# Kernel optimization log

Hardware: AMD Instinct MI355X
Metric: run time of the kernel (lower is better)

## Reference

```python
import jax, jax.numpy as jnp
import numpy as np

NUM_BINS = 64
MAX_DIST = 25.0
HIDDEN = 256
B = 64        # number of graphs
S = 1024      # points per graph (setup builds equal-size contiguous segments)
EPS = 1e-8


def setup_inputs() -> dict:
    key = jax.random.key(0)
    k1, k2, k3, k4, k5 = jax.random.split(key, 5)
    N = B * S
    # scale positions so pairwise distances spread across [0, 25] bins
    pos = jax.random.normal(k1, (N, 3), dtype=jnp.float32) * 5.0
    batch = jnp.repeat(jnp.arange(B, dtype=jnp.int32), S)  # sorted graph ids
    # nn.Linear params, torch convention W:[out,in]
    W1 = jax.random.normal(k2, (HIDDEN, NUM_BINS), dtype=jnp.float32) / np.sqrt(NUM_BINS)
    b1 = jax.random.normal(k3, (HIDDEN,), dtype=jnp.float32) * 0.01
    W2 = jax.random.normal(k4, (HIDDEN, HIDDEN), dtype=jnp.float32) / np.sqrt(HIDDEN)
    b2 = jax.random.normal(k5, (HIDDEN,), dtype=jnp.float32) * 0.01
    return {"pos": pos, "W1": W1, "b1": b1, "W2": W2, "b2": b2, "batch": batch}


def _histograms(pos, batch):
    # batch ids are contiguous equal-size segments -> reshape into [B,S,3]
    p = pos.reshape(B, S, 3)
    # pairwise distances per graph via gram trick (matches torch.cdist)
    sq = jnp.sum(p * p, axis=-1)                                  # [B,S]
    d2 = sq[:, :, None] + sq[:, None, :] - 2.0 * jnp.einsum("bsd,btd->bst", p, p)
    dist = jnp.sqrt(jnp.maximum(d2, 0.0))                         # [B,S,S]
    triu = jnp.triu(jnp.ones((S, S), dtype=bool), k=1)            # i<j pairs
    # histc semantics: values in [0, MAX_DIST] counted, value==MAX_DIST -> last bin
    valid = triu[None] & (dist <= MAX_DIST)
    bins = jnp.clip(jnp.floor(dist * (NUM_BINS / MAX_DIST)).astype(jnp.int32), 0, NUM_BINS - 1)
    ids = (jnp.arange(B, dtype=jnp.int32)[:, None, None] * NUM_BINS + bins).reshape(-1)
    hist = jax.ops.segment_sum(valid.astype(jnp.float32).reshape(-1), ids,
                               num_segments=B * NUM_BINS).reshape(B, NUM_BINS)
    return hist / (jnp.sum(hist, axis=-1, keepdims=True) + EPS)


def reference(pos, W1, b1, W2, b2, batch):
    hist = _histograms(pos, batch)                                # [B, NUM_BINS]
    h = jax.nn.silu(hist @ W1.T + b1)                             # [B, HIDDEN]
    return h @ W2.T + b2                                          # [B, HIDDEN]
```

## Files before the change

### kernel.cpp

```cpp
#include <hip/hip_runtime.h>

#define NBINS 64
#define NGRAPH 64
#define SPTS 1024
#define HID 256
#define TILE 128
#define NPAIR 36
#define BPG NPAIR
#define NSUB 8
#define NBINT 65

__device__ __constant__ unsigned char ti_tab[NPAIR] = {
  0,0,0,0,0,0,0,0, 1,1,1,1,1,1,1, 2,2,2,2,2,2, 3,3,3,3,3, 4,4,4,4, 5,5,5, 6,6, 7};
__device__ __constant__ unsigned char tj_tab[NPAIR] = {
  0,1,2,3,4,5,6,7, 1,2,3,4,5,6,7, 2,3,4,5,6,7, 3,4,5,6,7, 4,5,6,7, 5,6,7, 6,7, 7};

template <bool OFFDIAG>
__device__ __forceinline__ void pair_loop(const float4* __restrict__ plj,
                                          unsigned int* __restrict__ h8,
                                          float4 pa, float4 pb, int il0, int il1,
                                          int jbase, unsigned int sub) {
  #pragma unroll 8
  for (int jj = 0; jj < 32; ++jj) {
    int jl = jbase + jj;
    float4 pj = plj[jl];
    float dxa = pa.x - pj.x, dya = pa.y - pj.y, dza = pa.z - pj.z;
    float d2a = dxa * dxa + dya * dya + dza * dza;
    float dxb = pb.x - pj.x, dyb = pb.y - pj.y, dzb = pb.z - pj.z;
    float d2b = dxb * dxb + dyb * dyb + dzb * dzb;
    unsigned int ia = (unsigned int)(int)__builtin_amdgcn_sqrtf(d2a);
    unsigned int ib = (unsigned int)(int)__builtin_amdgcn_sqrtf(d2b);
    ia = ia > 64u ? 64u : ia;
    ib = ib > 64u ? 64u : ib;
    if (!OFFDIAG) {
      ia = (il0 < jl) ? ia : 64u;
      ib = (il1 < jl) ? ib : 64u;
    }
    atomicAdd(&h8[ia * NSUB + sub], 1u);
    atomicAdd(&h8[ib * NSUB + sub], 1u);
  }
}

__global__ __launch_bounds__(256) void hist_kernel(const float* __restrict__ pos,
                                                   unsigned int* __restrict__ partial) {
  int bid = blockIdx.x;
  int g   = bid / NPAIR;
  int p   = bid - g * NPAIR;
  int ti  = ti_tab[p];
  int tj  = tj_tab[p];
  int t   = threadIdx.x;
  const float S = 2.56f;

  __shared__ float4 plj[TILE];
  __shared__ unsigned int h8[NBINT * NSUB];

  h8[t] = 0u;
  h8[t + 256] = 0u;
  if (t < NBINT * NSUB - 512) h8[t + 512] = 0u;
  if (t < TILE) {
    const float* gp = pos + (size_t)((g << 10) + (tj << 7) + t) * 3;
    plj[t] = make_float4(gp[0] * S, gp[1] * S, gp[2] * S, 0.0f);
  }

  int il0 = (t & 63) * 2;
  int il1 = il0 + 1;
  const float* ip = pos + (size_t)((g << 10) + (ti << 7) + il0) * 3;
  float4 pa = make_float4(ip[0] * S, ip[1] * S, ip[2] * S, 0.0f);
  float4 pb = make_float4(ip[3] * S, ip[4] * S, ip[5] * S, 0.0f);
  int jbase = (t >> 6) * 32;
  unsigned int sub = t & (NSUB - 1);
  __syncthreads();

  if (ti != tj) pair_loop<true >(plj, h8, pa, pb, il0, il1, jbase, sub);
  else          pair_loop<false>(plj, h8, pa, pb, il0, il1, jbase, sub);
  __syncthreads();

  if (t < NBINS) {
    unsigned int s = 0u;
    #pragma unroll
    for (int k = 0; k < NSUB; ++k) s += h8[t * NSUB + k];
    partial[(size_t)bid * NBINS + t] = s;
  }
}

__global__ __launch_bounds__(256) void mlp_kernel(const unsigned int* __restrict__ partial,
                                                  const float* __restrict__ W1,
                                                  const float* __restrict__ b1,
                                                  const float* __restrict__ W2,
                                                  const float* __restrict__ b2,
                                                  float* __restrict__ out) {
  int g = blockIdx.x >> 2;
  int q = blockIdx.x & 3;
  int t = threadIdx.x;
  __shared__ float hn[NBINS];
  __shared__ float h1[HID];
  __shared__ float p2[4][NBINS];

  if (t < NBINS) {
    unsigned int s = 0u;
    const unsigned int* pp = partial + (size_t)g * BPG * NBINS + t;
    #pragma unroll
    for (int p = 0; p < BPG; ++p) s += pp[p * NBINS];
    float hv = (float)s;
    float tot = hv;
    #pragma unroll
    for (int m = 1; m < 64; m <<= 1) tot += __shfl_xor(tot, m, 64);
    hn[t] = hv / (tot + 1e-8f);
  }
  __syncthreads();

  {
    float acc = b1[t];
    const float4* w = (const float4*)(W1 + (size_t)t * NBINS);
    #pragma unroll
    for (int k = 0; k < NBINS / 4; ++k) {
      float4 wv = w[k];
      acc += hn[4 * k] * wv.x + hn[4 * k + 1] * wv.y +
             hn[4 * k + 2] * wv.z + hn[4 * k + 3] * wv.w;
    }
    float sig = 1.0f / (1.0f + expf(-acc));
    h1[t] = acc * sig;
  }
  __syncthreads();

  {
    int o  = (q << 6) + (t & 63);
    int ks = (t >> 6) << 6;
    float acc = 0.0f;
    const float4* w = (const float4*)(W2 + (size_t)o * HID + ks);
    #pragma unroll
    for (int k = 0; k < 16; ++k) {
      float4 wv = w[k];
      acc += h1[ks + 4 * k] * wv.x + h1[ks + 4 * k + 1] * wv.y +
             h1[ks + 4 * k + 2] * wv.z + h1[ks + 4 * k + 3] * wv.w;
    }
    p2[t >> 6][t & 63] = acc;
  }
  __syncthreads();

  if (t < 64) {
    int o = (q << 6) + t;
    out[(size_t)g * HID + o] = b2[o] + p2[0][t] + p2[1][t] + p2[2][t] + p2[3][t];
  }
}

extern "C" void kernel_launch(void* const* d_in, const int* in_sizes, int n_in,
                              void* d_out, int out_size, void* d_ws, size_t ws_size,
                              hipStream_t stream) {
  const float* pos = (const float*)d_in[0];
  const float* W1  = (const float*)d_in[1];
  const float* b1  = (const float*)d_in[2];
  const float* W2  = (const float*)d_in[3];
  const float* b2  = (const float*)d_in[4];

  unsigned int* partial = (unsigned int*)d_ws;

  hipLaunchKernelGGL(hist_kernel, dim3(NGRAPH * BPG), dim3(256), 0, stream, pos, partial);
  hipLaunchKernelGGL(mlp_kernel, dim3(NGRAPH * 4), dim3(256), 0, stream,
                     partial, W1, b1, W2, b2, (float*)d_out);
}
```

Measured before the change: 85.13 us.

## Fuse histogram and MLP via last-block-arrives pattern with wider LDS sub-histograms

Merges the histogram and MLP kernels into one launch: each block atomically adds its partial histogram into a global per-graph histogram, and the last block to arrive for a graph, detected with an arrival counter, runs the MLP for that graph. Shared-memory sub-histograms grow from 8 interleaved copies to 32 padded per-wavefront copies to cut atomic contention and bank conflicts. The second MLP layer now has each thread compute one full output row, where before the work was split across four blocks per graph. The change adds a memset launch and fences, and the serial per-graph MLP in a single block may lengthen the tail.

```diff
diff --git a/kernel.cpp b/kernel.cpp
--- a/kernel.cpp
+++ b/kernel.cpp
@@ -2,13 +2,11 @@
 
 #define NBINS 64
 #define NGRAPH 64
-#define SPTS 1024
 #define HID 256
 #define TILE 128
 #define NPAIR 36
-#define BPG NPAIR
-#define NSUB 8
-#define NBINT 65
+#define NSUB 32
+#define HSTR 65
 
 __device__ __constant__ unsigned char ti_tab[NPAIR] = {
   0,0,0,0,0,0,0,0, 1,1,1,1,1,1,1, 2,2,2,2,2,2, 3,3,3,3,3, 4,4,4,4, 5,5,5, 6,6, 7};
@@ -17,9 +15,9 @@
 
 template <bool OFFDIAG>
 __device__ __forceinline__ void pair_loop(const float4* __restrict__ plj,
-                                          unsigned int* __restrict__ h8,
+                                          unsigned int* __restrict__ hw,
                                           float4 pa, float4 pb, int il0, int il1,
-                                          int jbase, unsigned int sub) {
+                                          int jbase) {
   #pragma unroll 8
   for (int jj = 0; jj < 32; ++jj) {
     int jl = jbase + jj;
@@ -36,13 +34,18 @@
       ia = (il0 < jl) ? ia : 64u;
       ib = (il1 < jl) ? ib : 64u;
     }
-    atomicAdd(&h8[ia * NSUB + sub], 1u);
-    atomicAdd(&h8[ib * NSUB + sub], 1u);
+    atomicAdd(&hw[ia], 1u);
+    atomicAdd(&hw[ib], 1u);
   }
 }
 
-__global__ __launch_bounds__(256) void hist_kernel(const float* __restrict__ pos,
-                                                   unsigned int* __restrict__ partial) {
+__global__ __launch_bounds__(256) void fused_kernel(
+    const float* __restrict__ pos,
+    const float* __restrict__ W1, const float* __restrict__ b1,
+    const float* __restrict__ W2, const float* __restrict__ b2,
+    unsigned int* __restrict__ ghist,
+    unsigned int* __restrict__ cnt,
+    float* __restrict__ out) {
   int bid = blockIdx.x;
   int g   = bid / NPAIR;
   int p   = bid - g * NPAIR;
@@ -52,11 +55,12 @@
   const float S = 2.56f;
 
   __shared__ float4 plj[TILE];
-  __shared__ unsigned int h8[NBINT * NSUB];
+  __shared__ unsigned int h[NSUB * HSTR];
+  __shared__ float hn[NBINS];
+  __shared__ float h1[HID];
+  __shared__ unsigned int arrival;
 
-  h8[t] = 0u;
-  h8[t + 256] = 0u;
-  if (t < NBINT * NSUB - 512) h8[t + 512] = 0u;
+  for (int k = t; k < NSUB * HSTR; k += 256) h[k] = 0u;
   if (t < TILE) {
     const float* gp = pos + (size_t)((g << 10) + (tj << 7) + t) * 3;
     plj[t] = make_float4(gp[0] * S, gp[1] * S, gp[2] * S, 0.0f);
@@ -68,39 +72,29 @@
   float4 pa = make_float4(ip[0] * S, ip[1] * S, ip[2] * S, 0.0f);
   float4 pb = make_float4(ip[3] * S, ip[4] * S, ip[5] * S, 0.0f);
   int jbase = (t >> 6) * 32;
-  unsigned int sub = t & (NSUB - 1);
+  unsigned int* hw = h + ((t >> 6) * 8 + (t & 7)) * HSTR;
   __syncthreads();
 
-  if (ti != tj) pair_loop<true >(plj, h8, pa, pb, il0, il1, jbase, sub);
-  else          pair_loop<false>(plj, h8, pa, pb, il0, il1, jbase, sub);
+  if (ti != tj) pair_loop<true >(plj, hw, pa, pb, il0, il1, jbase);
+  else          pair_loop<false>(plj, hw, pa, pb, il0, il1, jbase);
   __syncthreads();
 
   if (t < NBINS) {
     unsigned int s = 0u;
     #pragma unroll
-    for (int k = 0; k < NSUB; ++k) s += h8[t * NSUB + k];
-    partial[(size_t)bid * NBINS + t] = s;
+    for (int k = 0; k < NSUB; ++k) s += h[k * HSTR + t];
+    atomicAdd(&ghist[g * NBINS + t], s);
   }
-}
-
-__global__ __launch_bounds__(256) void mlp_kernel(const unsigned int* __restrict__ partial,
-                                                  const float* __restrict__ W1,
-                                                  const float* __restrict__ b1,
-                                                  const float* __restrict__ W2,
-                                                  const float* __restrict__ b2,
-                                                  float* __restrict__ out) {
-  int g = blockIdx.x >> 2;
-  int q = blockIdx.x & 3;
-  int t = threadIdx.x;
-  __shared__ float hn[NBINS];
-  __shared__ float h1[HID];
-  __shared__ float p2[4][NBINS];
+  __threadfence();
+  __syncthreads();
+  if (t == 0) arrival = atomicAdd(&cnt[g], 1u);
+  __syncthreads();
+  if (arrival != NPAIR - 1) return;
+  __threadfence();
 
   if (t < NBINS) {
-    unsigned int s = 0u;
-    const unsigned int* pp = partial + (size_t)g * BPG * NBINS + t;
-    #pragma unroll
-    for (int p = 0; p < BPG; ++p) s += pp[p * NBINS];
+    unsigned int s = __hip_atomic_load(&ghist[g * NBINS + t],
+                                       __ATOMIC_RELAXED, __HIP_MEMORY_SCOPE_AGENT);
     float hv = (float)s;
     float tot = hv;
     #pragma unroll
@@ -124,23 +118,15 @@
   __syncthreads();
 
   {
-    int o  = (q << 6) + (t & 63);
-    int ks = (t >> 6) << 6;
-    float acc = 0.0f;
-    const float4* w = (const float4*)(W2 + (size_t)o * HID + ks);
-    #pragma unroll
-    for (int k = 0; k < 16; ++k) {
+    float ax = 0.f, ay = 0.f, az = 0.f, aw = 0.f;
+    const float4* w = (const float4*)(W2 + (size_t)t * HID);
+    #pragma unroll 8
+    for (int k = 0; k < HID / 4; ++k) {
       float4 wv = w[k];
-      acc += h1[ks + 4 * k] * wv.x + h1[ks + 4 * k + 1] * wv.y +
-             h1[ks + 4 * k + 2] * wv.z + h1[ks + 4 * k + 3] * wv.w;
+      ax += h1[4 * k] * wv.x;  ay += h1[4 * k + 1] * wv.y;
+      az += h1[4 * k + 2] * wv.z;  aw += h1[4 * k + 3] * wv.w;
     }
-    p2[t >> 6][t & 63] = acc;
-  }
-  __syncthreads();
-
-  if (t < 64) {
-    int o = (q << 6) + t;
-    out[(size_t)g * HID + o] = b2[o] + p2[0][t] + p2[1][t] + p2[2][t] + p2[3][t];
+    out[(size_t)g * HID + t] = b2[t] + ((ax + ay) + (az + aw));
   }
 }
 
@@ -153,9 +139,10 @@
   const float* W2  = (const float*)d_in[3];
   const float* b2  = (const float*)d_in[4];
 
-  unsigned int* partial = (unsigned int*)d_ws;
+  unsigned int* ghist = (unsigned int*)d_ws;
+  unsigned int* cnt   = ghist + NGRAPH * NBINS;
+  hipMemsetAsync(d_ws, 0, (NGRAPH * NBINS + NGRAPH) * sizeof(unsigned int), stream);
 
-  hipLaunchKernelGGL(hist_kernel, dim3(NGRAPH * BPG), dim3(256), 0, stream, pos, partial);
-  hipLaunchKernelGGL(mlp_kernel, dim3(NGRAPH * 4), dim3(256), 0, stream,
-                     partial, W1, b1, W2, b2, (float*)d_out);
+  hipLaunchKernelGGL(fused_kernel, dim3(NGRAPH * NPAIR), dim3(256), 0, stream,
+                     pos, W1, b1, W2, b2, ghist, cnt, (float*)d_out);
 }
```

After: 258.9 us. +204.1%, slower.
